# Optimization experiments

Hardware: AMD Instinct MI355X
Metric: run time of the kernel (lower is better)

Reference implementation:

```python
import jax, jax.numpy as jnp
import numpy as np

N_NODES = 50000
N_EDGES = 800000
IN_F, OUT_F, N_HEADS = 128, 64, 4
NEG_SLOPE = 0.2
EPS = 1e-12


def setup_inputs() -> dict:
    key = jax.random.key(0)
    ks = jax.random.split(key, 6)
    x = jax.random.normal(ks[0], (N_NODES, IN_F), dtype=jnp.float32)
    edge_index = jax.random.randint(ks[1], (2, N_EDGES), 0, N_NODES, dtype=jnp.int32)
    # xavier-uniform-like scaled params
    W = jax.random.normal(ks[2], (IN_F, OUT_F), dtype=jnp.float32) * (2.0 / (IN_F + OUT_F)) ** 0.5
    a_l = jax.random.normal(ks[3], (OUT_F, N_HEADS), dtype=jnp.float32) * (2.0 / (OUT_F + N_HEADS)) ** 0.5
    a_r = jax.random.normal(ks[4], (OUT_F, N_HEADS), dtype=jnp.float32) * (2.0 / (OUT_F + N_HEADS)) ** 0.5
    b = jnp.zeros((OUT_F,), dtype=jnp.float32)
    return {"x": x, "edge_index": edge_index, "W": W, "a_l": a_l, "a_r": a_r, "b": b}


def reference(x, edge_index, W, a_l, a_r, b):
    # GATConv forward (eval mode: attn dropout is identity).
    # Dense NxNxH scatter + L1 normalize in the original == per-row edge softmax
    # over exp(leaky_relu(el[row]+er[col])); honor edge sparsity directly.
    n = x.shape[0]
    h = x @ W                      # [N, D] node representations
    el = h @ a_l                   # [N, H] left (dst/row) scores
    er = h @ a_r                   # [N, H] right (src/col) scores
    row, col = edge_index[0], edge_index[1]
    e = el[row] + er[col]          # [E, H]
    e = jnp.where(e > 0, e, NEG_SLOPE * e)   # leaky_relu(0.2)
    e = jnp.exp(e)
    denom = jax.ops.segment_sum(e, row, num_segments=n)        # [N, H]
    attn = e / jnp.maximum(denom[row], EPS)                    # [E, H] L1-normalized per row
    msg = attn[:, :, None] * h[col][:, None, :]                # [E, H, D]
    out = jax.ops.segment_sum(msg, row, num_segments=n)        # [N, H, D]
    out = out + b                                              # bias broadcast over heads
    return out.reshape(n, -1)                                  # [N, H*D]
```

## Files before the change

### kernel.cpp

```cpp
#include <hip/hip_runtime.h>

#define N_NODES 50000
#define N_EDGES 800000
#define IN_F    128
#define OUT_F   64
#define N_HEADS 4
#define NEG_SLOPE 0.2f
#define EPS 1e-12f

#define NODE_BLOCKS 782
#define NB    391
#define CHUNK 2048
#define NCH   391
#define S2N   (NB * NCH)
#define S2B   150

typedef __attribute__((ext_vector_type(8))) short bf16x8;
typedef __attribute__((ext_vector_type(4))) float f32x4;

__device__ __forceinline__ unsigned short f2bf(float f) {
    unsigned int u = __float_as_uint(f);
    u += 0x7FFFu + ((u >> 16) & 1u);
    return (unsigned short)(u >> 16);
}

__global__ __launch_bounds__(256) void k_init(
    const float* __restrict__ W, unsigned short* __restrict__ Wt,
    const int* __restrict__ row, int* __restrict__ histG)
{
    __shared__ int hist[NB];
    const int bb = blockIdx.x;
    const int t = threadIdx.x;
    if (bb < 4) {
        int i = bb * 256 + t;
        for (; i < OUT_F * IN_F; i += 4 * 256) {
            int c = i >> 7, k = i & 127;
            Wt[i] = f2bf(W[k * OUT_F + c]);
        }
        return;
    }
    const int ch = bb - 4;
    for (int i = t; i < NB; i += 256) hist[i] = 0;
    __syncthreads();
    const int e0 = ch * CHUNK + t * 8;
    if (e0 + 7 < N_EDGES) {
        int4 a = *(const int4*)(row + e0);
        int4 c = *(const int4*)(row + e0 + 4);
        atomicAdd(&hist[a.x >> 7], 1); atomicAdd(&hist[a.y >> 7], 1);
        atomicAdd(&hist[a.z >> 7], 1); atomicAdd(&hist[a.w >> 7], 1);
        atomicAdd(&hist[c.x >> 7], 1); atomicAdd(&hist[c.y >> 7], 1);
        atomicAdd(&hist[c.z >> 7], 1); atomicAdd(&hist[c.w >> 7], 1);
    } else {
        #pragma unroll
        for (int j = 0; j < 8; ++j)
            if (e0 + j < N_EDGES) atomicAdd(&hist[row[e0 + j] >> 7], 1);
    }
    __syncthreads();
    for (int i = t; i < NB; i += 256) histG[i * NCH + ch] = hist[i];
}

__global__ __launch_bounds__(256) void k_h_el_er(
    const float* __restrict__ x, const unsigned short* __restrict__ Wt,
    const float* __restrict__ a_l, const float* __restrict__ a_r,
    unsigned short* __restrict__ h_bf,
    float* __restrict__ el, float* __restrict__ er)
{
    __shared__ unsigned short xs[64 * 128];
    __shared__ unsigned short wsh[64 * 128];
    const int tid = threadIdx.x;
    const int node0 = blockIdx.x * 64;

    {
        const uint4* src = (const uint4*)Wt;
        #pragma unroll
        for (int j = 0; j < 4; ++j) {
            int idx = tid + 256 * j;
            int r = idx >> 4;
            int cb = (idx & 15) << 4;
            uint4 v = src[idx];
            *(uint4*)((char*)wsh + r * 256 + (cb ^ ((r & 7) << 4))) = v;
        }
    }
    {
        const int r = tid >> 2;
        const int c0 = (tid & 3) * 32;
        const int node = node0 + r;
        unsigned int pk[16];
        if (node < N_NODES) {
            const float* src = x + (size_t)node * IN_F + c0;
            #pragma unroll
            for (int i = 0; i < 8; ++i) {
                float4 v = *(const float4*)(src + 4 * i);
                pk[2 * i + 0] = (unsigned)f2bf(v.x) | ((unsigned)f2bf(v.y) << 16);
                pk[2 * i + 1] = (unsigned)f2bf(v.z) | ((unsigned)f2bf(v.w) << 16);
            }
        } else {
            #pragma unroll
            for (int i = 0; i < 16; ++i) pk[i] = 0;
        }
        #pragma unroll
        for (int q = 0; q < 4; ++q) {
            int cb = c0 * 2 + q * 16;
            *(uint4*)((char*)xs + r * 256 + (cb ^ ((r & 7) << 4))) =
                make_uint4(pk[4 * q], pk[4 * q + 1], pk[4 * q + 2], pk[4 * q + 3]);
        }
    }
    __syncthreads();

    const int w  = tid >> 6, l = tid & 63;
    const int lr = l & 15, lg = l >> 4;
    const int arow = w * 16 + lr;

    bf16x8 afr[4];
    #pragma unroll
    for (int t = 0; t < 4; ++t) {
        int cb = t * 64 + lg * 16;
        afr[t] = *(const bf16x8*)((char*)xs + arow * 256 + (cb ^ ((arow & 7) << 4)));
    }

    const f32x4 zero = {0.f, 0.f, 0.f, 0.f};
    f32x4 acc[4] = {zero, zero, zero, zero};
    #pragma unroll
    for (int nt = 0; nt < 4; ++nt) {
        const int brow = nt * 16 + lr;
        #pragma unroll
        for (int t = 0; t < 4; ++t) {
            int cb = t * 64 + lg * 16;
            bf16x8 bfr = *(const bf16x8*)((char*)wsh + brow * 256 + (cb ^ ((brow & 7) << 4)));
            acc[nt] = __builtin_amdgcn_mfma_f32_16x16x32_bf16(afr[t], bfr, acc[nt], 0, 0, 0);
        }
    }

    #pragma unroll
    for (int r = 0; r < 4; ++r) {
        const int node = node0 + w * 16 + lg * 4 + r;
        if (node < N_NODES) {
            #pragma unroll
            for (int nt = 0; nt < 4; ++nt)
                h_bf[(size_t)node * OUT_F + nt * 16 + lr] = f2bf(acc[nt][r]);
        }
    }

    float4 al4[4], ar4[4];
    #pragma unroll
    for (int nt = 0; nt < 4; ++nt) {
        al4[nt] = *(const float4*)(a_l + (size_t)(nt * 16 + lr) * N_HEADS);
        ar4[nt] = *(const float4*)(a_r + (size_t)(nt * 16 + lr) * N_HEADS);
    }
    #pragma unroll
    for (int r = 0; r < 4; ++r) {
        float4 pl = make_float4(0.f, 0.f, 0.f, 0.f);
        float4 pr = make_float4(0.f, 0.f, 0.f, 0.f);
        #pragma unroll
        for (int nt = 0; nt < 4; ++nt) {
            const float v = acc[nt][r];
            pl.x += v * al4[nt].x; pl.y += v * al4[nt].y;
            pl.z += v * al4[nt].z; pl.w += v * al4[nt].w;
            pr.x += v * ar4[nt].x; pr.y += v * ar4[nt].y;
            pr.z += v * ar4[nt].z; pr.w += v * ar4[nt].w;
        }
        #pragma unroll
        for (int off = 1; off < 16; off <<= 1) {
            pl.x += __shfl_xor(pl.x, off); pl.y += __shfl_xor(pl.y, off);
            pl.z += __shfl_xor(pl.z, off); pl.w += __shfl_xor(pl.w, off);
            pr.x += __shfl_xor(pr.x, off); pr.y += __shfl_xor(pr.y, off);
            pr.z += __shfl_xor(pr.z, off); pr.w += __shfl_xor(pr.w, off);
        }
        const int node = node0 + w * 16 + lg * 4 + r;
        if (lr == 0 && node < N_NODES) {
            *(float4*)(el + (size_t)node * N_HEADS) = pl;
            *(float4*)(er + (size_t)node * N_HEADS) = pr;
        }
    }
}

__global__ __launch_bounds__(256) void k_scan2_local(
    const int* __restrict__ histG, int* __restrict__ scanHist,
    int* __restrict__ blocksum)
{
    __shared__ int wsum[4];
    const int t = threadIdx.x;
    const int base = blockIdx.x * 1024 + t * 4;

    int4 d = make_int4(0, 0, 0, 0);
    if (base + 3 < S2N) d = *(const int4*)(histG + base);
    else {
        if (base + 0 < S2N) d.x = histG[base + 0];
        if (base + 1 < S2N) d.y = histG[base + 1];
        if (base + 2 < S2N) d.z = histG[base + 2];
        if (base + 3 < S2N) d.w = histG[base + 3];
    }
    const int tsum = d.x + d.y + d.z + d.w;

    const int lane = t & 63, wave = t >> 6;
    int inc = tsum;
    #pragma unroll
    for (int off = 1; off < 64; off <<= 1) {
        int v = __shfl_up(inc, off);
        if (lane >= off) inc += v;
    }
    if (lane == 63) wsum[wave] = inc;
    __syncthreads();

    int woff = 0;
    #pragma unroll
    for (int w = 0; w < 4; ++w) woff += (w < wave) ? wsum[w] : 0;

    const int ex = woff + inc - tsum;
    int4 o;
    o.x = ex; o.y = ex + d.x; o.z = o.y + d.y; o.w = o.z + d.z;
    if (base + 3 < S2N) *(int4*)(scanHist + base) = o;
    else {
        if (base + 0 < S2N) scanHist[base + 0] = o.x;
        if (base + 1 < S2N) scanHist[base + 1] = o.y;
        if (base + 2 < S2N) scanHist[base + 2] = o.z;
        if (base + 3 < S2N) scanHist[base + 3] = o.w;
    }
    if (t == 0) blocksum[blockIdx.x] = wsum[0] + wsum[1] + wsum[2] + wsum[3];
}

__global__ __launch_bounds__(256) void k_scan2_add(
    const int* __restrict__ blocksum, int* __restrict__ scanHist)
{
    const int bb = blockIdx.x;
    int off = 0;
    for (int i = 0; i < bb; ++i) off += blocksum[i];
    if (off == 0) return;

    const int t = threadIdx.x;
    const int base = bb * 1024 + t * 4;
    if (base + 3 < S2N) {
        int4 v = *(int4*)(scanHist + base);
        v.x += off; v.y += off; v.z += off; v.w += off;
        *(int4*)(scanHist + base) = v;
    } else {
        if (base + 0 < S2N) scanHist[base + 0] += off;
        if (base + 1 < S2N) scanHist[base + 1] += off;
        if (base + 2 < S2N) scanHist[base + 2] += off;
        if (base + 3 < S2N) scanHist[base + 3] += off;
    }
}

__global__ __launch_bounds__(256) void k_scatter(
    const int* __restrict__ row, const int* __restrict__ col,
    const int* __restrict__ scanHist, unsigned* __restrict__ ebuf)
{
    __shared__ int off[NB];
    const int ch = blockIdx.x;
    const int t = threadIdx.x;
    for (int i = t; i < NB; i += 256) off[i] = scanHist[i * NCH + ch];
    __syncthreads();
    const int e0 = ch * CHUNK;
    #pragma unroll
    for (int k = 0; k < 8; ++k) {
        const int e = e0 + t + k * 256;
        if (e < N_EDGES) {
            const int r = row[e], c = col[e];
            const int pos = atomicAdd(&off[r >> 7], 1);
            ebuf[pos] = ((unsigned)(r & 127) << 17) | (unsigned)c;
        }
    }
}

__global__ __launch_bounds__(256) void k_bucket(
    const unsigned* __restrict__ ebuf, const int* __restrict__ scanHist,
    const float* __restrict__ el, const float* __restrict__ er,
    int* __restrict__ rowptr, int* __restrict__ csr_col,
    float4* __restrict__ csr_w)
{
    __shared__ float4 elv[128];
    __shared__ int cnt[128];
    __shared__ int wsum2[2];
    const int b = blockIdx.x;
    const int t = threadIdx.x;
    const int node0 = b << 7;
    const int base = scanHist[b * NCH];
    const int end  = (b < NB - 1) ? scanHist[(b + 1) * NCH] : N_EDGES;

    if (t < 128) {
        const int node = node0 + t;
        elv[t] = (node < N_NODES) ? *(const float4*)(el + node * 4)
                                  : make_float4(0.f, 0.f, 0.f, 0.f);
        cnt[t] = 0;
    }
    __syncthreads();
    for (int i = base + t; i < end; i += 256)
        atomicAdd(&cnt[ebuf[i] >> 17], 1);
    __syncthreads();

    int inc = 0, val = 0;
    const int lane = t & 63, wave = t >> 6;
    if (t < 128) {
        val = cnt[t];
        inc = val;
        #pragma unroll
        for (int off = 1; off < 64; off <<= 1) {
            int v = __shfl_up(inc, off);
            if (lane >= off) inc += v;
        }
        if (lane == 63) wsum2[wave] = inc;
    }
    __syncthreads();
    int excl = 0;
    if (t < 128) {
        const int woff = (wave == 1) ? wsum2[0] : 0;
        excl = base + woff + inc - val;
        const int node = node0 + t;
        if (node < N_NODES) rowptr[node] = excl;
    }
    if (b == NB - 1 && t == 0) rowptr[N_NODES] = N_EDGES;
    __syncthreads();
    if (t < 128) cnt[t] = excl;
    __syncthreads();

    for (int i = base + t; i < end; i += 256) {
        const unsigned p = ebuf[i];
        const int r = p >> 17;
        const int c = (int)(p & 0x1FFFFu);
        const int pos = atomicAdd(&cnt[r], 1);
        const float4 e4 = elv[r];
        const float4 r4 = *(const float4*)(er + ((unsigned)c << 2));
        float s0 = e4.x + r4.x, s1 = e4.y + r4.y;
        float s2 = e4.z + r4.z, s3 = e4.w + r4.w;
        s0 = s0 > 0.f ? s0 : NEG_SLOPE * s0;
        s1 = s1 > 0.f ? s1 : NEG_SLOPE * s1;
        s2 = s2 > 0.f ? s2 : NEG_SLOPE * s2;
        s3 = s3 > 0.f ? s3 : NEG_SLOPE * s3;
        csr_col[pos] = c;
        csr_w[pos] = make_float4(__expf(s0), __expf(s1), __expf(s2), __expf(s3));
    }
}

__global__ __launch_bounds__(256) void k_gather(
    const int* __restrict__ rowptr, const int* __restrict__ csr_col,
    const float4* __restrict__ csr_w,
    const unsigned short* __restrict__ h_bf, const float* __restrict__ b,
    float* __restrict__ out)
{
    int n = blockIdx.x * 4 + (threadIdx.x >> 6);
    if (n >= N_NODES) return;
    const int lane = threadIdx.x & 63;
    const int g    = lane >> 4;
    const int fq   = lane & 15;

    const int s0 = rowptr[n], s1 = rowptr[n + 1];
    const int nit = (s1 - s0 + 3) >> 2;

    float acc[4][4];
    #pragma unroll
    for (int hd = 0; hd < 4; ++hd)
        #pragma unroll
        for (int f = 0; f < 4; ++f) acc[hd][f] = 0.f;
    float den[4] = {0.f, 0.f, 0.f, 0.f};

#define GLOAD(ii, WV, HV)                                                  \
    {                                                                      \
        WV = make_float4(0.f, 0.f, 0.f, 0.f);                              \
        HV = make_uint2(0u, 0u);                                           \
        const int j = s0 + (ii) * 4 + g;                                   \
        if ((ii) < nit && j < s1) {                                        \
            const int c = csr_col[j];                                      \
            WV = csr_w[j];                                                 \
            HV = *(const uint2*)(h_bf + (((unsigned)c << 6) + (fq << 2))); \
        }                                                                  \
    }

    float4 w0, w1; uint2 h0, h1;
    GLOAD(0, w0, h0);
    GLOAD(1, w1, h1);

    for (int it = 0; it < nit; ++it) {
        float4 w2; uint2 h2;
        GLOAD(it + 2, w2, h2);

        const float f0 = __uint_as_float(h0.x << 16);
        const float f1 = __uint_as_float(h0.x & 0xFFFF0000u);
        const float f2 = __uint_as_float(h0.y << 16);
        const float f3 = __uint_as_float(h0.y & 0xFFFF0000u);

        den[0] += w0.x; den[1] += w0.y; den[2] += w0.z; den[3] += w0.w;
        acc[0][0] += w0.x * f0; acc[0][1] += w0.x * f1; acc[0][2] += w0.x * f2; acc[0][3] += w0.x * f3;
        acc[1][0] += w0.y * f0; acc[1][1] += w0.y * f1; acc[1][2] += w0.y * f2; acc[1][3] += w0.y * f3;
        acc[2][0] += w0.z * f0; acc[2][1] += w0.z * f1; acc[2][2] += w0.z * f2; acc[2][3] += w0.z * f3;
        acc[3][0] += w0.w * f0; acc[3][1] += w0.w * f1; acc[3][2] += w0.w * f2; acc[3][3] += w0.w * f3;

        w0 = w1; h0 = h1;
        w1 = w2; h1 = h2;
    }
#undef GLOAD

    #pragma unroll
    for (int hd = 0; hd < 4; ++hd) {
        float v = den[hd];
        v += __shfl_xor(v, 16); v += __shfl_xor(v, 32);
        den[hd] = v;
        #pragma unroll
        for (int f = 0; f < 4; ++f) {
            float u = acc[hd][f];
            u += __shfl_xor(u, 16); u += __shfl_xor(u, 32);
            acc[hd][f] = u;
        }
    }

    const float dg = g == 0 ? den[0] : g == 1 ? den[1] : g == 2 ? den[2] : den[3];
    const float inv = 1.f / fmaxf(dg, EPS);
    float4 o;
    o.x = (g == 0 ? acc[0][0] : g == 1 ? acc[1][0] : g == 2 ? acc[2][0] : acc[3][0]);
    o.y = (g == 0 ? acc[0][1] : g == 1 ? acc[1][1] : g == 2 ? acc[2][1] : acc[3][1]);
    o.z = (g == 0 ? acc[0][2] : g == 1 ? acc[1][2] : g == 2 ? acc[2][2] : acc[3][2]);
    o.w = (g == 0 ? acc[0][3] : g == 1 ? acc[1][3] : g == 2 ? acc[2][3] : acc[3][3]);

    const float4 bias = *(const float4*)(b + fq * 4);
    o.x = o.x * inv + bias.x;
    o.y = o.y * inv + bias.y;
    o.z = o.z * inv + bias.z;
    o.w = o.w * inv + bias.w;
    *(float4*)(out + (size_t)n * (N_HEADS * OUT_F) + g * 64 + fq * 4) = o;
}

extern "C" void kernel_launch(void* const* d_in, const int* in_sizes, int n_in,
                              void* d_out, int out_size, void* d_ws, size_t ws_size,
                              hipStream_t stream)
{
    const float* x   = (const float*)d_in[0];
    const int*   ei  = (const int*)d_in[1];
    const float* W   = (const float*)d_in[2];
    const float* a_l = (const float*)d_in[3];
    const float* a_r = (const float*)d_in[4];
    const float* b   = (const float*)d_in[5];
    float* out = (float*)d_out;

    char* ws = (char*)d_ws;
    unsigned short* h_bf = (unsigned short*)(ws);
    float*    el       = (float*)   (ws +  6400000);
    float*    er       = (float*)   (ws +  7200000);
    unsigned short* Wt = (unsigned short*)(ws + 8000000);
    int*      histG    = (int*)     (ws +  8016384);
    int*      scanHist = (int*)     (ws +  8627920);
    int*      blocksum = (int*)     (ws +  9239456);
    unsigned* ebuf     = (unsigned*)(ws +  9240480);
    int*      csr_col  = (int*)     (ws + 12440480);
    float4*   csr_w    = (float4*)  (ws + 15640496);
    int*      rowptr   = (int*)     (ws + 28440496);

    const int* row = ei;
    const int* col = ei + N_EDGES;

    k_init       <<<4 + NCH, 256, 0, stream>>>(W, Wt, row, histG);
    k_h_el_er    <<<NODE_BLOCKS, 256, 0, stream>>>(x, Wt, a_l, a_r, h_bf, el, er);
    k_scan2_local<<<S2B, 256, 0, stream>>>(histG, scanHist, blocksum);
    k_scan2_add  <<<S2B, 256, 0, stream>>>(blocksum, scanHist);
    k_scatter    <<<NCH, 256, 0, stream>>>(row, col, scanHist, ebuf);
    k_bucket     <<<NB, 256, 0, stream>>>(ebuf, scanHist, el, er, rowptr, csr_col, csr_w);
    k_gather     <<<N_NODES / 4, 256, 0, stream>>>(rowptr, csr_col, csr_w, h_bf, b, out);
}
```

Measured before the change: 92.81 us.

## Pack CSR edge col and bf16 weights into one uint4, widen gather and chunks

Merges the separate CSR column array and fp32 float4 weight array into one 16-byte record per edge holding the column and four bf16 attention weights. Each gather lane now processes two edges per iteration with a one-stage prefetch. Histogram and scatter chunks double in size, which halves the chunk count and the scan work. The intent is fewer memory transactions and less scan and launch overhead, at the cost of bf16 precision on the attention weights and an unused padding word per record.

```diff
diff --git a/kernel.cpp b/kernel.cpp
--- a/kernel.cpp
+++ b/kernel.cpp
@@ -10,10 +10,10 @@
 
 #define NODE_BLOCKS 782
 #define NB    391
-#define CHUNK 2048
-#define NCH   391
+#define CHUNK 4096
+#define NCH   196
 #define S2N   (NB * NCH)
-#define S2B   150
+#define S2B   75
 
 typedef __attribute__((ext_vector_type(8))) short bf16x8;
 typedef __attribute__((ext_vector_type(4))) float f32x4;
@@ -23,6 +23,8 @@
     u += 0x7FFFu + ((u >> 16) & 1u);
     return (unsigned short)(u >> 16);
 }
+__device__ __forceinline__ float bf_lo(unsigned u) { return __uint_as_float(u << 16); }
+__device__ __forceinline__ float bf_hi(unsigned u) { return __uint_as_float(u & 0xFFFF0000u); }
 
 __global__ __launch_bounds__(256) void k_init(
     const float* __restrict__ W, unsigned short* __restrict__ Wt,
@@ -42,18 +44,19 @@
     const int ch = bb - 4;
     for (int i = t; i < NB; i += 256) hist[i] = 0;
     __syncthreads();
-    const int e0 = ch * CHUNK + t * 8;
-    if (e0 + 7 < N_EDGES) {
-        int4 a = *(const int4*)(row + e0);
-        int4 c = *(const int4*)(row + e0 + 4);
-        atomicAdd(&hist[a.x >> 7], 1); atomicAdd(&hist[a.y >> 7], 1);
-        atomicAdd(&hist[a.z >> 7], 1); atomicAdd(&hist[a.w >> 7], 1);
-        atomicAdd(&hist[c.x >> 7], 1); atomicAdd(&hist[c.y >> 7], 1);
-        atomicAdd(&hist[c.z >> 7], 1); atomicAdd(&hist[c.w >> 7], 1);
-    } else {
-        #pragma unroll
-        for (int j = 0; j < 8; ++j)
-            if (e0 + j < N_EDGES) atomicAdd(&hist[row[e0 + j] >> 7], 1);
+    const int e0 = ch * CHUNK + t * 16;
+    #pragma unroll
+    for (int q = 0; q < 4; ++q) {
+        const int e = e0 + q * 4;
+        if (e + 3 < N_EDGES) {
+            int4 a = *(const int4*)(row + e);
+            atomicAdd(&hist[a.x >> 7], 1); atomicAdd(&hist[a.y >> 7], 1);
+            atomicAdd(&hist[a.z >> 7], 1); atomicAdd(&hist[a.w >> 7], 1);
+        } else {
+            #pragma unroll
+            for (int j = 0; j < 4; ++j)
+                if (e + j < N_EDGES) atomicAdd(&hist[row[e + j] >> 7], 1);
+        }
     }
     __syncthreads();
     for (int i = t; i < NB; i += 256) histG[i * NCH + ch] = hist[i];
@@ -252,7 +255,7 @@
     __syncthreads();
     const int e0 = ch * CHUNK;
     #pragma unroll
-    for (int k = 0; k < 8; ++k) {
+    for (int k = 0; k < 16; ++k) {
         const int e = e0 + t + k * 256;
         if (e < N_EDGES) {
             const int r = row[e], c = col[e];
@@ -265,8 +268,7 @@
 __global__ __launch_bounds__(256) void k_bucket(
     const unsigned* __restrict__ ebuf, const int* __restrict__ scanHist,
     const float* __restrict__ el, const float* __restrict__ er,
-    int* __restrict__ rowptr, int* __restrict__ csr_col,
-    float4* __restrict__ csr_w)
+    int* __restrict__ rowptr, uint4* __restrict__ edata)
 {
     __shared__ float4 elv[128];
     __shared__ int cnt[128];
@@ -326,14 +328,14 @@
         s1 = s1 > 0.f ? s1 : NEG_SLOPE * s1;
         s2 = s2 > 0.f ? s2 : NEG_SLOPE * s2;
         s3 = s3 > 0.f ? s3 : NEG_SLOPE * s3;
-        csr_col[pos] = c;
-        csr_w[pos] = make_float4(__expf(s0), __expf(s1), __expf(s2), __expf(s3));
+        const unsigned w01 = (unsigned)f2bf(__expf(s0)) | ((unsigned)f2bf(__expf(s1)) << 16);
+        const unsigned w23 = (unsigned)f2bf(__expf(s2)) | ((unsigned)f2bf(__expf(s3)) << 16);
+        edata[pos] = make_uint4((unsigned)c, w01, w23, 0u);
     }
 }
 
 __global__ __launch_bounds__(256) void k_gather(
-    const int* __restrict__ rowptr, const int* __restrict__ csr_col,
-    const float4* __restrict__ csr_w,
+    const int* __restrict__ rowptr, const uint4* __restrict__ edata,
     const unsigned short* __restrict__ h_bf, const float* __restrict__ b,
     float* __restrict__ out)
 {
@@ -344,7 +346,7 @@
     const int fq   = lane & 15;
 
     const int s0 = rowptr[n], s1 = rowptr[n + 1];
-    const int nit = (s1 - s0 + 3) >> 2;
+    const int nit = (s1 - s0 + 7) >> 3;
 
     float acc[4][4];
     #pragma unroll
@@ -353,41 +355,51 @@
         for (int f = 0; f < 4; ++f) acc[hd][f] = 0.f;
     float den[4] = {0.f, 0.f, 0.f, 0.f};
 
-#define GLOAD(ii, WV, HV)                                                  \
-    {                                                                      \
-        WV = make_float4(0.f, 0.f, 0.f, 0.f);                              \
-        HV = make_uint2(0u, 0u);                                           \
-        const int j = s0 + (ii) * 4 + g;                                   \
-        if ((ii) < nit && j < s1) {                                        \
-            const int c = csr_col[j];                                      \
-            WV = csr_w[j];                                                 \
-            HV = *(const uint2*)(h_bf + (((unsigned)c << 6) + (fq << 2))); \
-        }                                                                  \
-    }
-
-    float4 w0, w1; uint2 h0, h1;
-    GLOAD(0, w0, h0);
-    GLOAD(1, w1, h1);
-
-    for (int it = 0; it < nit; ++it) {
-        float4 w2; uint2 h2;
-        GLOAD(it + 2, w2, h2);
-
-        const float f0 = __uint_as_float(h0.x << 16);
-        const float f1 = __uint_as_float(h0.x & 0xFFFF0000u);
-        const float f2 = __uint_as_float(h0.y << 16);
-        const float f3 = __uint_as_float(h0.y & 0xFFFF0000u);
-
-        den[0] += w0.x; den[1] += w0.y; den[2] += w0.z; den[3] += w0.w;
-        acc[0][0] += w0.x * f0; acc[0][1] += w0.x * f1; acc[0][2] += w0.x * f2; acc[0][3] += w0.x * f3;
-        acc[1][0] += w0.y * f0; acc[1][1] += w0.y * f1; acc[1][2] += w0.y * f2; acc[1][3] += w0.y * f3;
-        acc[2][0] += w0.z * f0; acc[2][1] += w0.z * f1; acc[2][2] += w0.z * f2; acc[2][3] += w0.z * f3;
-        acc[3][0] += w0.w * f0; acc[3][1] += w0.w * f1; acc[3][2] += w0.w * f2; acc[3][3] += w0.w * f3;
-
-        w0 = w1; h0 = h1;
-        w1 = w2; h1 = h2;
-    }
-#undef GLOAD
+    if (nit > 0) {
+#define LOADE(ii, E0, E1)                                   \
+        {                                                   \
+            const int j0 = s0 + (ii) * 8 + 2 * g;           \
+            const int j1 = j0 + 1;                          \
+            E0 = edata[j0 < s1 ? j0 : s1 - 1];              \
+            E1 = edata[j1 < s1 ? j1 : s1 - 1];              \
+            if (j0 >= s1) { E0.y = 0u; E0.z = 0u; }         \
+            if (j1 >= s1) { E1.y = 0u; E1.z = 0u; }         \
+        }
+#define LOADH(E, H)                                                              \
+        H = *(const uint2*)(h_bf + (((E.x & 0xFFFFu) << 6) + ((unsigned)fq << 2)));
+#define COMP1(E, H)                                                              \
+        {                                                                        \
+            const float w0 = bf_lo(E.y), w1 = bf_hi(E.y);                        \
+            const float w2 = bf_lo(E.z), w3 = bf_hi(E.z);                        \
+            const float f0 = bf_lo(H.x), f1 = bf_hi(H.x);                        \
+            const float f2 = bf_lo(H.y), f3 = bf_hi(H.y);                        \
+            den[0] += w0; den[1] += w1; den[2] += w2; den[3] += w3;              \
+            acc[0][0] += w0 * f0; acc[0][1] += w0 * f1;                          \
+            acc[0][2] += w0 * f2; acc[0][3] += w0 * f3;                          \
+            acc[1][0] += w1 * f0; acc[1][1] += w1 * f1;                          \
+            acc[1][2] += w1 * f2; acc[1][3] += w1 * f3;                          \
+            acc[2][0] += w2 * f0; acc[2][1] += w2 * f1;                          \
+            acc[2][2] += w2 * f2; acc[2][3] += w2 * f3;                          \
+            acc[3][0] += w3 * f0; acc[3][1] += w3 * f1;                          \
+            acc[3][2] += w3 * f2; acc[3][3] += w3 * f3;                          \
+        }
+
+        uint4 a0, a1, b0, b1;
+        uint2 ha0, ha1, hb0, hb1;
+        LOADE(0, a0, a1);
+        LOADH(a0, ha0); LOADH(a1, ha1);
+
+        for (int it = 0; it < nit; ++it) {
+            LOADE(it + 1, b0, b1);
+            LOADH(b0, hb0); LOADH(b1, hb1);
+            COMP1(a0, ha0);
+            COMP1(a1, ha1);
+            a0 = b0; a1 = b1; ha0 = hb0; ha1 = hb1;
+        }
+#undef LOADE
+#undef LOADH
+#undef COMP1
+    }
 
     #pragma unroll
     for (int hd = 0; hd < 4; ++hd) {
@@ -436,12 +448,11 @@
     float*    er       = (float*)   (ws +  7200000);
     unsigned short* Wt = (unsigned short*)(ws + 8000000);
     int*      histG    = (int*)     (ws +  8016384);
-    int*      scanHist = (int*)     (ws +  8627920);
-    int*      blocksum = (int*)     (ws +  9239456);
-    unsigned* ebuf     = (unsigned*)(ws +  9240480);
-    int*      csr_col  = (int*)     (ws + 12440480);
-    float4*   csr_w    = (float4*)  (ws + 15640496);
-    int*      rowptr   = (int*)     (ws + 28440496);
+    int*      scanHist = (int*)     (ws +  8322928);
+    int*      blocksum = (int*)     (ws +  8629472);
+    unsigned* ebuf     = (unsigned*)(ws +  8630496);
+    int*      rowptr   = (int*)     (ws + 11830496);
+    uint4*    edata    = (uint4*)   (ws + 12030512);
 
     const int* row = ei;
     const int* col = ei + N_EDGES;
@@ -451,6 +462,6 @@
     k_scan2_local<<<S2B, 256, 0, stream>>>(histG, scanHist, blocksum);
     k_scan2_add  <<<S2B, 256, 0, stream>>>(blocksum, scanHist);
     k_scatter    <<<NCH, 256, 0, stream>>>(row, col, scanHist, ebuf);
-    k_bucket     <<<NB, 256, 0, stream>>>(ebuf, scanHist, el, er, rowptr, csr_col, csr_w);
-    k_gather     <<<N_NODES / 4, 256, 0, stream>>>(rowptr, csr_col, csr_w, h_bf, b, out);
-}
+    k_bucket     <<<NB, 256, 0, stream>>>(ebuf, scanHist, el, er, rowptr, edata);
+    k_gather     <<<N_NODES / 4, 256, 0, stream>>>(rowptr, edata, h_bf, b, out);
+}
```

Result: faster. 85.48 us (-7.9%).
